# Kernel optimization log

Hardware: AMD Instinct MI355X
Metric: run time of the kernel (lower is better)

Reference implementation:

```python
import jax, jax.numpy as jnp
import numpy as np

N, D, H, L, E, P = 50000, 128, 128, 3, 640000, 100000


def setup_inputs() -> dict:
    key = jax.random.key(0)
    ks = jax.random.split(key, 10)
    x = jax.random.normal(ks[0], (N, D), dtype=jnp.float32)
    ei = jax.random.randint(ks[1], (2, E), 0, N, dtype=jnp.int64)
    pos = jax.random.randint(ks[2], (2, P), 0, N, dtype=jnp.int64)
    neg = jax.random.randint(ks[3], (2, P), 0, N, dtype=jnp.int64)
    # GCN weights: layer0 is [D,H], rest [H,H]; D==H so stack as [L,H,H]
    gcn_w = jax.random.normal(ks[4], (L, H, H), dtype=jnp.float32) / np.sqrt(H)
    gcn_b = jnp.zeros((L, H), dtype=jnp.float32)
    pred_w = jax.random.normal(ks[5], (H * L, 1), dtype=jnp.float32) / np.sqrt(H * L)
    pred_b = jnp.zeros((1,), dtype=jnp.float32)
    return {"x": x, "ei": ei, "pos": pos, "neg": neg,
            "gcn_w": gcn_w, "gcn_b": gcn_b, "pred_w": pred_w, "pred_b": pred_b}


def reference(x, ei, pos, neg, gcn_w, gcn_b, pred_w, pred_b):
    n = x.shape[0]
    loops = jnp.arange(n, dtype=ei.dtype)
    src = jnp.concatenate([ei[0], loops])  # self-loops (GCNConv default)
    dst = jnp.concatenate([ei[1], loops])
    deg = jax.ops.segment_sum(jnp.ones_like(dst, dtype=x.dtype), dst, num_segments=n)
    dinv = jax.lax.rsqrt(deg)  # deg >= 1 thanks to self-loops
    coef = (dinv[src] * dinv[dst])[:, None]  # [E+N, 1] symmetric norm

    embs = []
    h = x
    for i in range(gcn_w.shape[0]):
        hw = h @ gcn_w[i]                                   # [N, H]
        agg = jax.ops.segment_sum(hw[src] * coef, dst, num_segments=n)
        h = jax.nn.relu(agg + gcn_b[i])
        embs.append(h)
    z = jnp.concatenate(embs, axis=1)                        # [N, H*L]

    def logits(e):
        return (z[e[0]] * z[e[1]]) @ pred_w + pred_b         # [P, 1]

    pos_logit = logits(pos)
    neg_logit = logits(neg)
    # BCEWithLogitsLoss with targets [1...1, 0...0], mean reduction
    total = pos_logit.shape[0] + neg_logit.shape[0]
    loss = (jnp.sum(-jax.nn.log_sigmoid(pos_logit)) +
            jnp.sum(-jax.nn.log_sigmoid(-neg_logit))) / total
    return loss
```

## Files before the change

### kernel.cpp

```cpp
#include <hip/hip_runtime.h>
#include <hip/hip_bf16.h>

#define DD 128

typedef __attribute__((ext_vector_type(8))) short short8;
typedef __attribute__((ext_vector_type(4))) float f32x4;
typedef __attribute__((ext_vector_type(2))) float f32x2;

static __device__ __forceinline__ int gtid() {
    return blockIdx.x * blockDim.x + threadIdx.x;
}

static __device__ __forceinline__ ushort f2bfu(float f) {
    __hip_bfloat16 h = __float2bfloat16(f);
    return *reinterpret_cast<ushort*>(&h);
}

static __device__ __forceinline__ unsigned int fp8e(float f) {
    unsigned int s = (__float_as_uint(f) >> 31) << 7;
    float a = fabsf(f);
    if (a < 0.015625f) return s | (unsigned int)rintf(a * 512.0f);
    unsigned int u = __float_as_uint(a);
    u += 0x0007FFFFu + ((u >> 20) & 1u);
    unsigned int e8 = (u >> 23) - 120u;
    unsigned int m = (u >> 20) & 7u;
    if (e8 > 15u || (e8 == 15u && m == 7u)) return s | 0x7Eu;
    return s | (e8 << 3) | m;
}

static __device__ __forceinline__ float fp8d(unsigned int b) {
    unsigned int t = b & 0x7Fu;
    float v = (t >= 8u) ? __uint_as_float((t << 20) + 0x3C000000u)
                        : (float)t * 0.001953125f;
    return (b & 0x80u) ? -v : v;
}

static __device__ __forceinline__ unsigned int pk8x4(float a, float b, float c, float d) {
#if __has_builtin(__builtin_amdgcn_cvt_pk_fp8_f32)
    int v = __builtin_amdgcn_cvt_pk_fp8_f32(a, b, 0, false);
    v = __builtin_amdgcn_cvt_pk_fp8_f32(c, d, v, true);
    return (unsigned int)v;
#else
    return fp8e(a) | (fp8e(b) << 8) | (fp8e(c) << 16) | (fp8e(d) << 24);
#endif
}

static __device__ __forceinline__ unsigned int pk8x2(float a, float b) {
#if __has_builtin(__builtin_amdgcn_cvt_pk_fp8_f32)
    return (unsigned int)__builtin_amdgcn_cvt_pk_fp8_f32(a, b, 0, false);
#else
    return fp8e(a) | (fp8e(b) << 8);
#endif
}

static __device__ __forceinline__ void fp8x4_dec(unsigned int u, float* f) {
#if __has_builtin(__builtin_amdgcn_cvt_pk_f32_fp8)
    f32x2 lo = __builtin_amdgcn_cvt_pk_f32_fp8((int)u, false);
    f32x2 hi = __builtin_amdgcn_cvt_pk_f32_fp8((int)u, true);
    f[0] = lo[0]; f[1] = lo[1]; f[2] = hi[0]; f[3] = hi[1];
#else
    f[0] = fp8d(u & 0xFFu);
    f[1] = fp8d((u >> 8) & 0xFFu);
    f[2] = fp8d((u >> 16) & 0xFFu);
    f[3] = fp8d((u >> 24) & 0xFFu);
#endif
}


__global__ void count_kernel(int* __restrict__ counts, const int* __restrict__ dst, int e) {
    int i = gtid();
    if (i < e) atomicAdd(&counts[dst[i]], 1);
}

__global__ void dinv_kernel(float* __restrict__ dinv, const int* __restrict__ counts, int n) {
    int i = gtid();
    if (i < n) dinv[i] = rsqrtf(1.0f + (float)counts[i]);
}

__global__ __launch_bounds__(256) void scan_blocks(const int* __restrict__ counts,
                                                   int* __restrict__ rowptr,
                                                   int* __restrict__ partial, int n) {
    __shared__ int s[256];
    int i = blockIdx.x * 256 + threadIdx.x;
    int v = (i < n) ? counts[i] : 0;
    s[threadIdx.x] = v;
    __syncthreads();
    for (int off = 1; off < 256; off <<= 1) {
        int t = (threadIdx.x >= off) ? s[threadIdx.x - off] : 0;
        __syncthreads();
        s[threadIdx.x] += t;
        __syncthreads();
    }
    if (i < n) rowptr[i] = s[threadIdx.x] - v;
    if (threadIdx.x == 255) partial[blockIdx.x] = s[255];
}

__global__ __launch_bounds__(256) void scan_partials(int* __restrict__ partial,
                                                     int* __restrict__ partial2, int nb) {
    __shared__ int s[256];
    int v = (threadIdx.x < nb) ? partial[threadIdx.x] : 0;
    s[threadIdx.x] = v;
    __syncthreads();
    for (int off = 1; off < 256; off <<= 1) {
        int t = (threadIdx.x >= off) ? s[threadIdx.x - off] : 0;
        __syncthreads();
        s[threadIdx.x] += t;
        __syncthreads();
    }
    partial2[threadIdx.x] = s[threadIdx.x] - v;
}

__global__ __launch_bounds__(256) void add_offsets(int* __restrict__ rowptr,
                                                   int* __restrict__ cursor,
                                                   const int* __restrict__ partial2,
                                                   int n, int e) {
    int i = blockIdx.x * 256 + threadIdx.x;
    if (i < n) {
        int r = rowptr[i] + partial2[blockIdx.x];
        rowptr[i] = r;
        cursor[i] = r;
        if (i == n - 1) rowptr[n] = e;
    }
}

__global__ void fill_kernel(const int* __restrict__ ei, int* __restrict__ cursor,
                            int* __restrict__ csr_src, int e) {
    int i = gtid();
    if (i >= e) return;
    int s = ei[i];
    int d = ei[e + i];
    int pos = atomicAdd(&cursor[d], 1);
    __builtin_nontemporal_store(s, &csr_src[pos]);
}

__global__ void cvt_kernel(const float* __restrict__ x, __hip_bfloat16* __restrict__ xh, size_t m) {
    size_t i = (size_t)blockIdx.x * blockDim.x + threadIdx.x;
    if (i < m) xh[i] = __float2bfloat16(x[i]);
}

__global__ __launch_bounds__(256) void wpack_kernel(const float* __restrict__ gcn_w,
                                                    ushort* __restrict__ wfrag) {
    int tid = blockIdx.x * 256 + threadIdx.x;
    if (tid >= 3 * 4 * 8 * 64) return;
    int lane = tid & 63;
    int c = (tid >> 6) & 7;
    int s = (tid >> 9) & 3;
    int l = tid >> 11;
    const float* W = gcn_w + (size_t)l * 128 * 128;
    int col = c * 16 + (lane & 15);
    int k0 = s * 32 + (lane >> 4) * 8;
    ushort u[8];
#pragma unroll
    for (int j = 0; j < 8; ++j) {
        u[j] = f2bfu(W[(size_t)(k0 + j) * 128 + col]);
    }
    *reinterpret_cast<uint4*>(wfrag + (size_t)tid * 8) = *reinterpret_cast<const uint4*>(u);
}


__global__ __launch_bounds__(256) void aggregate_bf16_kernel(
    const ushort* __restrict__ src, const int* __restrict__ rowptr,
    const int* __restrict__ csr_src, const float* __restrict__ dinv,
    ushort* __restrict__ aggh, int n) {
    int gid = gtid();
    int row = gid >> 6;
    if (row >= n) return;
    int lane = threadIdx.x & 63;
    int g = lane >> 4;
    int c = lane & 15;
    int j0 = rowptr[row], j1 = rowptr[row + 1];
    float dr = dinv[row];
    float acc[8] = {0.f, 0.f, 0.f, 0.f, 0.f, 0.f, 0.f, 0.f};
    for (int j = j0 + g; j < j1; j += 4) {
        int s = csr_src[j];
        float cf = dinv[s] * dr;
        uint4 v = *reinterpret_cast<const uint4*>(src + (size_t)s * 128 + c * 8);
        const unsigned int* u = (const unsigned int*)&v;
#pragma unroll
        for (int q = 0; q < 4; ++q) {
            acc[2 * q] = fmaf(cf, __uint_as_float(u[q] << 16), acc[2 * q]);
            acc[2 * q + 1] = fmaf(cf, __uint_as_float(u[q] & 0xffff0000u), acc[2 * q + 1]);
        }
    }
#pragma unroll
    for (int k = 0; k < 8; ++k) {
        acc[k] += __shfl_xor(acc[k], 16);
        acc[k] += __shfl_xor(acc[k], 32);
    }
    float d2 = dr * dr;
    uint4 sv = *reinterpret_cast<const uint4*>(src + (size_t)row * 128 + c * 8);
    const unsigned int* su = (const unsigned int*)&sv;
#pragma unroll
    for (int q = 0; q < 4; ++q) {
        acc[2 * q] = fmaf(d2, __uint_as_float(su[q] << 16), acc[2 * q]);
        acc[2 * q + 1] = fmaf(d2, __uint_as_float(su[q] & 0xffff0000u), acc[2 * q + 1]);
    }
    if (g == 0) {
        unsigned int pk[4];
#pragma unroll
        for (int q = 0; q < 4; ++q) {
            pk[q] = (unsigned int)f2bfu(acc[2 * q]) | ((unsigned int)f2bfu(acc[2 * q + 1]) << 16);
        }
        *reinterpret_cast<uint4*>(aggh + (size_t)row * 128 + c * 8) =
            *reinterpret_cast<const uint4*>(pk);
    }
}

__global__ __launch_bounds__(256) void aggregate_fp8_kernel(
    const unsigned char* __restrict__ srcq, const int* __restrict__ rowptr,
    const int* __restrict__ csr_src, const float* __restrict__ dinv,
    ushort* __restrict__ aggh, int n) {
    int gid = gtid();
    int row = gid >> 6;
    if (row >= n) return;
    int lane = threadIdx.x & 63;
    int g = lane >> 4;
    int c = lane & 15;
    int j0 = rowptr[row], j1 = rowptr[row + 1];
    float dr = dinv[row];
    float acc[8] = {0.f, 0.f, 0.f, 0.f, 0.f, 0.f, 0.f, 0.f};
    for (int j = j0 + g; j < j1; j += 4) {
        int s = csr_src[j];
        float cf = dinv[s] * dr;
        uint2 v = *reinterpret_cast<const uint2*>(srcq + (size_t)s * 384 + c * 8);
        float f[8];
        fp8x4_dec(v.x, f);
        fp8x4_dec(v.y, f + 4);
#pragma unroll
        for (int k = 0; k < 8; ++k) acc[k] = fmaf(cf, f[k], acc[k]);
    }
#pragma unroll
    for (int k = 0; k < 8; ++k) {
        acc[k] += __shfl_xor(acc[k], 16);
        acc[k] += __shfl_xor(acc[k], 32);
    }
    float d2 = dr * dr;
    uint2 sv = *reinterpret_cast<const uint2*>(srcq + (size_t)row * 384 + c * 8);
    float sf[8];
    fp8x4_dec(sv.x, sf);
    fp8x4_dec(sv.y, sf + 4);
#pragma unroll
    for (int k = 0; k < 8; ++k) acc[k] = fmaf(d2, sf[k], acc[k]);
    if (g == 0) {
        unsigned int pk[4];
#pragma unroll
        for (int q = 0; q < 4; ++q) {
            pk[q] = (unsigned int)f2bfu(acc[2 * q]) | ((unsigned int)f2bfu(acc[2 * q + 1]) << 16);
        }
        *reinterpret_cast<uint4*>(aggh + (size_t)row * 128 + c * 8) =
            *reinterpret_cast<const uint4*>(pk);
    }
}

__global__ __launch_bounds__(256) void gemm_mfma_kernel(
    const ushort* __restrict__ aggh, const ushort* __restrict__ wfrag,
    const float* __restrict__ bias, const float* __restrict__ pwsl,
    unsigned char* __restrict__ zq_sl, unsigned char* __restrict__ zqw_sl, int ntiles) {
    int lane = threadIdx.x & 63;
    int wv = threadIdx.x >> 6;
    short8 b0[4], b1[4];
    int c0 = wv * 2;
#pragma unroll
    for (int s = 0; s < 4; ++s) {
        b0[s] = *reinterpret_cast<const short8*>(wfrag + ((size_t)(s * 8 + c0) * 64 + lane) * 8);
        b1[s] = *reinterpret_cast<const short8*>(wfrag + ((size_t)(s * 8 + c0 + 1) * 64 + lane) * 8);
    }
    int rlo = lane & 15;
    int kg = lane >> 4;
    int col0 = wv * 32 + rlo;
    int col1 = col0 + 16;
    float bias0 = bias[col0], bias1 = bias[col1];
    float pw0 = pwsl[col0] * 8.0f, pw1 = pwsl[col1] * 8.0f;
    for (int rt = blockIdx.x; rt < ntiles; rt += gridDim.x) {
        const ushort* ap = aggh + (size_t)(rt * 16 + rlo) * 128 + kg * 8;
        short8 a0 = *reinterpret_cast<const short8*>(ap);
        short8 a1 = *reinterpret_cast<const short8*>(ap + 32);
        short8 a2 = *reinterpret_cast<const short8*>(ap + 64);
        short8 a3 = *reinterpret_cast<const short8*>(ap + 96);
        f32x4 acc0 = {0.f, 0.f, 0.f, 0.f};
        f32x4 acc1 = {0.f, 0.f, 0.f, 0.f};
        acc0 = __builtin_amdgcn_mfma_f32_16x16x32_bf16(a0, b0[0], acc0, 0, 0, 0);
        acc1 = __builtin_amdgcn_mfma_f32_16x16x32_bf16(a0, b1[0], acc1, 0, 0, 0);
        acc0 = __builtin_amdgcn_mfma_f32_16x16x32_bf16(a1, b0[1], acc0, 0, 0, 0);
        acc1 = __builtin_amdgcn_mfma_f32_16x16x32_bf16(a1, b1[1], acc1, 0, 0, 0);
        acc0 = __builtin_amdgcn_mfma_f32_16x16x32_bf16(a2, b0[2], acc0, 0, 0, 0);
        acc1 = __builtin_amdgcn_mfma_f32_16x16x32_bf16(a2, b1[2], acc1, 0, 0, 0);
        acc0 = __builtin_amdgcn_mfma_f32_16x16x32_bf16(a3, b0[3], acc0, 0, 0, 0);
        acc1 = __builtin_amdgcn_mfma_f32_16x16x32_bf16(a3, b1[3], acc1, 0, 0, 0);
        int row0 = rt * 16 + kg * 4;
#pragma unroll
        for (int r = 0; r < 4; ++r) {
            float v0 = fmaxf(acc0[r] + bias0, 0.f);
            float v1 = fmaxf(acc1[r] + bias1, 0.f);
            unsigned int q = pk8x2(v0, v1);
            unsigned char* zr = zq_sl + (size_t)(row0 + r) * 384 + col0;
            zr[0] = (unsigned char)(q & 0xFFu);
            zr[16] = (unsigned char)((q >> 8) & 0xFFu);
            unsigned int w = pk8x2(v0 * pw0, v1 * pw1);
            unsigned char* wr = zqw_sl + (size_t)(row0 + r) * 384 + col0;
            wr[0] = (unsigned char)(w & 0xFFu);
            wr[16] = (unsigned char)((w >> 8) & 0xFFu);
        }
    }
}

__global__ __launch_bounds__(256) void loss_mfma_kernel(
    const unsigned char* __restrict__ zq, const unsigned char* __restrict__ zqw,
    const int* __restrict__ pos, const int* __restrict__ neg,
    const float* __restrict__ pb, float* __restrict__ partialOut,
    int p, float inv_total) {
    __shared__ float red[4];
    int lane = threadIdx.x & 63;
    int wv = threadIdx.x >> 6;
    int pairBase = (blockIdx.x * 4 + wv) * 16;
    float term = 0.f;
    if (pairBase < 2 * p) {
        int m = lane & 15;
        int kg = lane >> 4;
        int pi = pairBase + m;
        int pic = (pi < 2 * p) ? pi : (2 * p - 1);
        bool isneg = (pic >= p);
        const int* pr = isneg ? neg : pos;
        int idx = isneg ? (pic - p) : pic;
        int a = pr[idx];
        int b = pr[p + idx];
        const long* pa = reinterpret_cast<const long*>(zq + (size_t)a * 384) + kg;
        const long* pbw = reinterpret_cast<const long*>(zqw + (size_t)b * 384) + kg;
        long av[12], bv[12];
#pragma unroll
        for (int s = 0; s < 12; ++s) av[s] = pa[s * 4];
#pragma unroll
        for (int s = 0; s < 12; ++s) bv[s] = pbw[s * 4];
        f32x4 acc = {0.f, 0.f, 0.f, 0.f};
#pragma unroll
        for (int s = 0; s < 12; ++s) {
            acc = __builtin_amdgcn_mfma_f32_16x16x32_fp8_fp8(av[s], bv[s], acc, 0, 0, 0);
        }
        bool isdiag = (lane >> 4) == ((lane & 15) >> 2);
        int r2 = lane & 3;
        float v = (r2 == 0) ? acc[0] : (r2 == 1) ? acc[1] : (r2 == 2) ? acc[2] : acc[3];
        if (isdiag && pi < 2 * p) {
            float logit = v * 0.125f + pb[0];
            float t = isneg ? logit : -logit;
            term = (fmaxf(t, 0.f) + log1pf(expf(-fabsf(t)))) * inv_total;
        }
    }
#pragma unroll
    for (int off = 1; off < 64; off <<= 1) term += __shfl_xor(term, off);
    if (lane == 0) red[wv] = term;
    __syncthreads();
    if (threadIdx.x == 0) partialOut[blockIdx.x] = red[0] + red[1] + red[2] + red[3];
}

__global__ __launch_bounds__(256) void loss_reduce_kernel(
    const float* __restrict__ partial, float* __restrict__ out, int m) {
    __shared__ float s[256];
    float a = 0.f;
    for (int i = threadIdx.x; i < m; i += 256) a += partial[i];
    s[threadIdx.x] = a;
    __syncthreads();
    for (int off = 128; off > 0; off >>= 1) {
        if (threadIdx.x < off) s[threadIdx.x] += s[threadIdx.x + off];
        __syncthreads();
    }
    if (threadIdx.x == 0) out[0] = s[0];
}

extern "C" void kernel_launch(void* const* d_in, const int* in_sizes, int n_in,
                              void* d_out, int out_size, void* d_ws, size_t ws_size,
                              hipStream_t stream) {
    const float* x      = (const float*)d_in[0];
    const int*   ei     = (const int*)d_in[1];
    const int*   pos    = (const int*)d_in[2];
    const int*   neg    = (const int*)d_in[3];
    const float* gcn_w  = (const float*)d_in[4];
    const float* gcn_b  = (const float*)d_in[5];
    const float* pred_w = (const float*)d_in[6];
    const float* pred_b = (const float*)d_in[7];
    float* out = (float*)d_out;

    const int n = in_sizes[0] / DD;
    const int e = in_sizes[1] / 2;
    const int p = in_sizes[2] / 2;
    const int nb = (n + 255) / 256;

    char* ws = (char*)d_ws;
    size_t off = 0;
    auto alloc = [&](size_t bytes) {
        void* ptr = ws + off;
        off += (bytes + 255) & ~(size_t)255;
        return ptr;
    };
    float* dinv      = (float*)alloc((size_t)n * 4);
    int*   counts    = (int*)alloc((size_t)n * 4);
    int*   rowptr    = (int*)alloc((size_t)(n + 1) * 4);
    int*   cursor    = (int*)alloc((size_t)n * 4);
    int*   partial   = (int*)alloc(256 * 4);
    int*   partial2  = (int*)alloc(256 * 4);
    float* lossPart  = (float*)alloc((size_t)4096 * 4);
    int*   csr_src   = (int*)alloc((size_t)e * 4);
    ushort* wfrag    = (ushort*)alloc((size_t)3 * 2048 * 8 * 2);
    ushort* xh   = (ushort*)alloc((size_t)n * 128 * 2);
    ushort* aggh = (ushort*)alloc((size_t)n * 128 * 2);
    unsigned char* zq  = (unsigned char*)alloc((size_t)n * 384);
    unsigned char* zqw = (unsigned char*)alloc((size_t)n * 384);
    (void)ws_size;

    hipMemsetAsync(counts, 0, (size_t)n * 4, stream);

    count_kernel<<<(e + 255) / 256, 256, 0, stream>>>(counts, ei + e, e);
    dinv_kernel<<<nb, 256, 0, stream>>>(dinv, counts, n);
    scan_blocks<<<nb, 256, 0, stream>>>(counts, rowptr, partial, n);
    scan_partials<<<1, 256, 0, stream>>>(partial, partial2, nb);
    add_offsets<<<nb, 256, 0, stream>>>(rowptr, cursor, partial2, n, e);
    fill_kernel<<<(e + 255) / 256, 256, 0, stream>>>(ei, cursor, csr_src, e);

    cvt_kernel<<<(int)(((size_t)n * 128 + 255) / 256), 256, 0, stream>>>(
        x, (__hip_bfloat16*)xh, (size_t)n * 128);
    wpack_kernel<<<24, 256, 0, stream>>>(gcn_w, wfrag);

    const int ntiles = n / 16;
    const int aggBlocks = (n * 64 + 255) / 256;
    for (int l = 0; l < 3; ++l) {
        if (l == 0) {
            aggregate_bf16_kernel<<<aggBlocks, 256, 0, stream>>>(
                xh, rowptr, csr_src, dinv, aggh, n);
        } else {
            aggregate_fp8_kernel<<<aggBlocks, 256, 0, stream>>>(
                zq + (size_t)(l - 1) * 128, rowptr, csr_src, dinv, aggh, n);
        }
        gemm_mfma_kernel<<<ntiles, 256, 0, stream>>>(
            aggh, wfrag + (size_t)l * 2048 * 8,
            gcn_b + (size_t)l * 128, pred_w + (size_t)l * 128,
            zq + (size_t)l * 128, zqw + (size_t)l * 128, ntiles);
    }

    float inv_total = 1.0f / (2.0f * (float)p);
    int lossBlocks = (2 * p + 63) / 64;
    loss_mfma_kernel<<<lossBlocks, 256, 0, stream>>>(
        zq, zqw, pos, neg, pred_b, lossPart, p, inv_total);
    loss_reduce_kernel<<<1, 256, 0, stream>>>(lossPart, out, lossBlocks);
}
```

Measured before the change: 285.7 us.

## Build CSR via coarse 64-row bins with shared-memory local sort

```diff
diff --git a/kernel.cpp b/kernel.cpp
--- a/kernel.cpp
+++ b/kernel.cpp
@@ -33,16 +33,6 @@
     float v = (t >= 8u) ? __uint_as_float((t << 20) + 0x3C000000u)
                         : (float)t * 0.001953125f;
     return (b & 0x80u) ? -v : v;
-}
-
-static __device__ __forceinline__ unsigned int pk8x4(float a, float b, float c, float d) {
-#if __has_builtin(__builtin_amdgcn_cvt_pk_fp8_f32)
-    int v = __builtin_amdgcn_cvt_pk_fp8_f32(a, b, 0, false);
-    v = __builtin_amdgcn_cvt_pk_fp8_f32(c, d, v, true);
-    return (unsigned int)v;
-#else
-    return fp8e(a) | (fp8e(b) << 8) | (fp8e(c) << 16) | (fp8e(d) << 24);
-#endif
 }
 
 static __device__ __forceinline__ unsigned int pk8x2(float a, float b) {
@@ -67,70 +57,89 @@
 }
 
 
-__global__ void count_kernel(int* __restrict__ counts, const int* __restrict__ dst, int e) {
+__global__ void bincount_kernel(const int* __restrict__ dst, int* __restrict__ binCounts, int e) {
     int i = gtid();
-    if (i < e) atomicAdd(&counts[dst[i]], 1);
-}
-
-__global__ void dinv_kernel(float* __restrict__ dinv, const int* __restrict__ counts, int n) {
-    int i = gtid();
-    if (i < n) dinv[i] = rsqrtf(1.0f + (float)counts[i]);
-}
-
-__global__ __launch_bounds__(256) void scan_blocks(const int* __restrict__ counts,
-                                                   int* __restrict__ rowptr,
-                                                   int* __restrict__ partial, int n) {
-    __shared__ int s[256];
-    int i = blockIdx.x * 256 + threadIdx.x;
-    int v = (i < n) ? counts[i] : 0;
-    s[threadIdx.x] = v;
-    __syncthreads();
-    for (int off = 1; off < 256; off <<= 1) {
-        int t = (threadIdx.x >= off) ? s[threadIdx.x - off] : 0;
+    if (i < e) atomicAdd(&binCounts[dst[i] >> 6], 1);
+}
+
+__global__ __launch_bounds__(1024) void binscan_kernel(
+    const int* __restrict__ binCounts, int* __restrict__ binptr, int* __restrict__ binCur,
+    int* __restrict__ rowptr, int m, int e, int n) {
+    __shared__ int s[1024];
+    int tid = threadIdx.x;
+    int v = (tid < m) ? binCounts[tid] : 0;
+    s[tid] = v;
+    __syncthreads();
+    for (int off = 1; off < 1024; off <<= 1) {
+        int t = (tid >= off) ? s[tid - off] : 0;
         __syncthreads();
-        s[threadIdx.x] += t;
+        s[tid] += t;
         __syncthreads();
     }
-    if (i < n) rowptr[i] = s[threadIdx.x] - v;
-    if (threadIdx.x == 255) partial[blockIdx.x] = s[255];
-}
-
-__global__ __launch_bounds__(256) void scan_partials(int* __restrict__ partial,
-                                                     int* __restrict__ partial2, int nb) {
-    __shared__ int s[256];
-    int v = (threadIdx.x < nb) ? partial[threadIdx.x] : 0;
-    s[threadIdx.x] = v;
-    __syncthreads();
-    for (int off = 1; off < 256; off <<= 1) {
-        int t = (threadIdx.x >= off) ? s[threadIdx.x - off] : 0;
-        __syncthreads();
-        s[threadIdx.x] += t;
-        __syncthreads();
-    }
-    partial2[threadIdx.x] = s[threadIdx.x] - v;
-}
-
-__global__ __launch_bounds__(256) void add_offsets(int* __restrict__ rowptr,
-                                                   int* __restrict__ cursor,
-                                                   const int* __restrict__ partial2,
-                                                   int n, int e) {
-    int i = blockIdx.x * 256 + threadIdx.x;
-    if (i < n) {
-        int r = rowptr[i] + partial2[blockIdx.x];
-        rowptr[i] = r;
-        cursor[i] = r;
-        if (i == n - 1) rowptr[n] = e;
-    }
-}
-
-__global__ void fill_kernel(const int* __restrict__ ei, int* __restrict__ cursor,
-                            int* __restrict__ csr_src, int e) {
+    if (tid < m) {
+        int ex = s[tid] - v;
+        binptr[tid] = ex;
+        binCur[tid] = ex;
+    }
+    if (tid == 0) {
+        binptr[m] = e;
+        rowptr[n] = e;
+    }
+}
+
+__global__ void binfill_kernel(const int* __restrict__ ei, int* __restrict__ binCur,
+                               uint2* __restrict__ binEdges, int e) {
     int i = gtid();
     if (i >= e) return;
     int s = ei[i];
     int d = ei[e + i];
-    int pos = atomicAdd(&cursor[d], 1);
-    __builtin_nontemporal_store(s, &csr_src[pos]);
+    int pos = atomicAdd(&binCur[d >> 6], 1);
+    uint2 ed;
+    ed.x = (unsigned int)s;
+    ed.y = (unsigned int)d;
+    binEdges[pos] = ed;
+}
+
+__global__ __launch_bounds__(256) void csr_from_bins_kernel(
+    const uint2* __restrict__ binEdges, const int* __restrict__ binptr,
+    int* __restrict__ rowptr, int* __restrict__ csr_src, int n) {
+    __shared__ int cnts[64];
+    __shared__ int curs[64];
+    int b = blockIdx.x;
+    int row0 = b << 6;
+    int base = binptr[b];
+    int cnt = binptr[b + 1] - base;
+    int tid = threadIdx.x;
+    if (tid < 64) cnts[tid] = 0;
+    __syncthreads();
+    for (int i = tid; i < cnt; i += 256) {
+        uint2 ed = binEdges[base + i];
+        atomicAdd(&cnts[ed.y - row0], 1);
+    }
+    __syncthreads();
+    if (tid < 64) {
+        int v = cnts[tid];
+        int inc = v;
+#pragma unroll
+        for (int off = 1; off < 64; off <<= 1) {
+            int t = __shfl_up(inc, off);
+            if (tid >= off) inc += t;
+        }
+        int ex = inc - v;
+        if (row0 + tid < n) rowptr[row0 + tid] = base + ex;
+        curs[tid] = ex;
+    }
+    __syncthreads();
+    for (int i = tid; i < cnt; i += 256) {
+        uint2 ed = binEdges[base + i];
+        int pos = base + atomicAdd(&curs[ed.y - row0], 1);
+        csr_src[pos] = (int)ed.x;
+    }
+}
+
+__global__ void dinv_kernel(float* __restrict__ dinv, const int* __restrict__ rowptr, int n) {
+    int i = gtid();
+    if (i < n) dinv[i] = rsqrtf(1.0f + (float)(rowptr[i + 1] - rowptr[i]));
 }
 
 __global__ void cvt_kernel(const float* __restrict__ x, __hip_bfloat16* __restrict__ xh, size_t m) {
@@ -382,7 +391,7 @@
     const int n = in_sizes[0] / DD;
     const int e = in_sizes[1] / 2;
     const int p = in_sizes[2] / 2;
-    const int nb = (n + 255) / 256;
+    const int nbins = (n + 63) >> 6;
 
     char* ws = (char*)d_ws;
     size_t off = 0;
@@ -392,13 +401,13 @@
         return ptr;
     };
     float* dinv      = (float*)alloc((size_t)n * 4);
-    int*   counts    = (int*)alloc((size_t)n * 4);
     int*   rowptr    = (int*)alloc((size_t)(n + 1) * 4);
-    int*   cursor    = (int*)alloc((size_t)n * 4);
-    int*   partial   = (int*)alloc(256 * 4);
-    int*   partial2  = (int*)alloc(256 * 4);
+    int*   binCounts = (int*)alloc((size_t)(nbins + 1) * 4);
+    int*   binptr    = (int*)alloc((size_t)(nbins + 1) * 4);
+    int*   binCur    = (int*)alloc((size_t)nbins * 4);
     float* lossPart  = (float*)alloc((size_t)4096 * 4);
     int*   csr_src   = (int*)alloc((size_t)e * 4);
+    uint2* binEdges  = (uint2*)alloc((size_t)e * 8);
     ushort* wfrag    = (ushort*)alloc((size_t)3 * 2048 * 8 * 2);
     ushort* xh   = (ushort*)alloc((size_t)n * 128 * 2);
     ushort* aggh = (ushort*)alloc((size_t)n * 128 * 2);
@@ -406,14 +415,13 @@
     unsigned char* zqw = (unsigned char*)alloc((size_t)n * 384);
     (void)ws_size;
 
-    hipMemsetAsync(counts, 0, (size_t)n * 4, stream);
-
-    count_kernel<<<(e + 255) / 256, 256, 0, stream>>>(counts, ei + e, e);
-    dinv_kernel<<<nb, 256, 0, stream>>>(dinv, counts, n);
-    scan_blocks<<<nb, 256, 0, stream>>>(counts, rowptr, partial, n);
-    scan_partials<<<1, 256, 0, stream>>>(partial, partial2, nb);
-    add_offsets<<<nb, 256, 0, stream>>>(rowptr, cursor, partial2, n, e);
-    fill_kernel<<<(e + 255) / 256, 256, 0, stream>>>(ei, cursor, csr_src, e);
+    hipMemsetAsync(binCounts, 0, (size_t)(nbins + 1) * 4, stream);
+
+    bincount_kernel<<<(e + 255) / 256, 256, 0, stream>>>(ei + e, binCounts, e);
+    binscan_kernel<<<1, 1024, 0, stream>>>(binCounts, binptr, binCur, rowptr, nbins, e, n);
+    binfill_kernel<<<(e + 255) / 256, 256, 0, stream>>>(ei, binCur, binEdges, e);
+    csr_from_bins_kernel<<<nbins, 256, 0, stream>>>(binEdges, binptr, rowptr, csr_src, n);
+    dinv_kernel<<<(n + 255) / 256, 256, 0, stream>>>(dinv, rowptr, n);
 
     cvt_kernel<<<(int)(((size_t)n * 128 + 255) / 256), 256, 0, stream>>>(
         x, (__hip_bfloat16*)xh, (size_t)n * 128);
```

Result: slower. 520.4 us (+82.1%).
